# Kernel tuning notes

Measured on AMD Instinct MI355X. Metric: run time of the kernel, lower is better.

The kernel has to match this reference:

```python
import jax, jax.numpy as jnp
import numpy as np

N = 50000       # nodes
E = 1600000     # edges (avg degree 32)
D = 128         # in = hidden = out channels
H = 4           # attention heads


def setup_inputs() -> dict:
    key = jax.random.key(0)
    ks = jax.random.split(key, 9)
    s = 1.0 / np.sqrt(D)  # ~kaiming-scale linear weights
    return {
        "x": jax.random.normal(ks[0], (N, D), jnp.float32),
        "Wk": jax.random.normal(ks[1], (D, D), jnp.float32) * s,
        "bk": jnp.zeros((D,), jnp.float32),
        "Wq": jax.random.normal(ks[2], (D, D), jnp.float32) * s,
        "bq": jnp.zeros((D,), jnp.float32),
        "Wv": jax.random.normal(ks[3], (D, D), jnp.float32) * s,
        "bv": jnp.zeros((D,), jnp.float32),
        "src": jax.random.randint(ks[4], (E,), 0, N, dtype=jnp.int32),
        "dst": jax.random.randint(ks[5], (E,), 0, N, dtype=jnp.int32),
    }


def reference(x, Wk, bk, Wq, bq, Wv, bv, src, dst):
    n = x.shape[0]
    heads = H
    dk = Wk.shape[0] // heads
    dv = Wv.shape[0] // heads
    # Dense projections (near-roofline GEMMs)
    k = (x @ Wk.T + bk).reshape(n, heads, dk)
    q = (x @ Wq.T + bq).reshape(n, heads, dk)
    v = (x @ Wv.T + bv).reshape(n, heads, dv)
    # u_dot_v: per-edge per-head dot product (NO 1/sqrt(dk) scaling in source)
    scores = jnp.einsum('ehd,ehd->eh', k[src], q[dst])  # [E,H]
    # edge_softmax: softmax over incoming edges of each destination node
    m = jax.ops.segment_max(scores, dst, num_segments=n)        # [N,H]
    p = jnp.exp(scores - m[dst])                                 # [E,H]
    denom = jax.ops.segment_sum(p, dst, num_segments=n)         # [N,H]
    alpha = p / denom[dst]                                       # [E,H]
    # u_mul_e + sum: weighted scatter-aggregation of source values
    res = jax.ops.segment_sum(v[src] * alpha[:, :, None], dst, num_segments=n)  # [N,H,dv]
    # original: view(batch_size, -1, out_channels) with batch_size = N -> [N,1,out]
    return res.reshape(n, 1, heads * dv)
```

## Files before the change

### kernel.cpp

```cpp
#include <hip/hip_runtime.h>
#include <hip/hip_bf16.h>
#include <hip/hip_fp16.h>

#define NN 50000
#define NE 1600000
#define DD 128
#define HH 4
#define BSH2 5
#define NBKT2 1563
#define NBP2 2048
#define CAP 1408
#define PCHUNK 8192
#define NPB 196
#define NGB 560
#define MIDB (NGB + NPB)

typedef __attribute__((ext_vector_type(8))) short short8;
typedef __attribute__((ext_vector_type(4))) float floatx4;
typedef __attribute__((ext_vector_type(2))) _Float16 h2;

__device__ inline h2 as_h2(unsigned u) {
    union { unsigned u; h2 h; } c; c.u = u; return c.h;
}

__device__ inline float dot4(h2 a01, h2 a23, h2 b01, h2 b23) {
#if defined(__has_builtin) && __has_builtin(__builtin_amdgcn_fdot2)
    return __builtin_amdgcn_fdot2(a01, b01, __builtin_amdgcn_fdot2(a23, b23, 0.f, false), false);
#else
    return (float)a01.x * (float)b01.x + (float)a01.y * (float)b01.y +
           (float)a23.x * (float)b23.x + (float)a23.y * (float)b23.y;
#endif
}

__global__ __launch_bounds__(256) void prep_w(
    const float* __restrict__ Wk, const float* __restrict__ Wq, const float* __restrict__ Wv,
    unsigned short* __restrict__ hi, unsigned short* __restrict__ lo, int* __restrict__ bcur)
{
    int j = blockIdx.x * 256 + threadIdx.x;
    if (j < NBP2) bcur[j] = 0;
    if (j >= 3 * DD * DD) return;
    int which = j / (DD * DD);
    int off = j - which * (DD * DD);
    const float* W = (which == 0) ? Wk : (which == 1) ? Wq : Wv;
    float w = W[off];
    unsigned int b = __float_as_uint(w);
    unsigned short h = (unsigned short)(b >> 16);
    float hf = __uint_as_float((unsigned int)h << 16);
    float l = w - hf;
    hi[j] = h;
    lo[j] = (unsigned short)(__float_as_uint(l) >> 16);
}

__global__ __launch_bounds__(256) void mid(
    const float* __restrict__ x,
    const unsigned short* __restrict__ whi, const unsigned short* __restrict__ wlo,
    const float* __restrict__ bk, const float* __restrict__ bq, const float* __restrict__ bv,
    uint2* __restrict__ kv2, uint4* __restrict__ qh4,
    const int* __restrict__ src, const int* __restrict__ dst,
    int* __restrict__ bcur, int* __restrict__ epack)
{
    __shared__ __align__(16) unsigned char smem[49152];

    if (blockIdx.x < NGB) {
        uint4* wl4 = (uint4*)smem;
        int tid = threadIdx.x;
        int wave = tid >> 6, lane = tid & 63;
        int m = lane & 15, quad = lane >> 4;
        unsigned short* st = (unsigned short*)(smem + 32768 + wave * 4096);
        uint4* st4 = (uint4*)st;
        uint2* st2 = (uint2*)st;

        for (int pp = 0; pp < 3; ++pp) {
            int wm = (pp == 0) ? 0 : (pp == 1) ? 2 : 1;
            const uint4* gh = (const uint4*)whi + (size_t)wm * 2048;
            __syncthreads();
            for (int g = tid; g < 2048; g += 256) {
                int l = (g & ~15) | ((g ^ (g >> 4)) & 15);
                wl4[l] = gh[g];
            }
            __syncthreads();
            const unsigned short* wloP = wlo + (size_t)wm * (DD * DD);
            const float* bias = (pp == 0) ? bk : (pp == 1) ? bv : bq;
            float bs[8];
#pragma unroll
            for (int ct = 0; ct < 8; ++ct) bs[ct] = bias[ct * 16 + m];

            for (int tile = blockIdx.x * 4 + wave; tile < 3125; tile += NGB * 4) {
                int n0 = tile * 16;
                const float* xrow = x + (size_t)(n0 + m) * DD + quad * 8;
                short8 ah[4], al[4];
#pragma unroll
                for (int ks = 0; ks < 4; ++ks) {
                    const float* xr = xrow + ks * 32;
                    float4 t0 = *(const float4*)xr;
                    float4 t1 = *(const float4*)(xr + 4);
                    float xv[8] = {t0.x, t0.y, t0.z, t0.w, t1.x, t1.y, t1.z, t1.w};
#pragma unroll
                    for (int j = 0; j < 8; ++j) {
                        unsigned int b = __float_as_uint(xv[j]);
                        unsigned short h = (unsigned short)(b >> 16);
                        float hf = __uint_as_float((unsigned int)h << 16);
                        float l = xv[j] - hf;
                        ah[ks][j] = (short)h;
                        al[ks][j] = (short)(__float_as_uint(l) >> 16);
                    }
                }

                floatx4 acc[8];
#pragma unroll
                for (int ct = 0; ct < 8; ++ct) acc[ct] = (floatx4){0.f, 0.f, 0.f, 0.f};

#pragma unroll
                for (int ks = 0; ks < 4; ++ks) {
#pragma unroll
                    for (int ct = 0; ct < 8; ++ct) {
                        int r = ct * 16 + m;
                        short8 bh = ((const short8*)wl4)[r * 16 + ((ks * 4 + quad) ^ m)];
                        short8 bl = *(const short8*)(wloP + (size_t)r * 128 + ks * 32 + quad * 8);
                        acc[ct] = __builtin_amdgcn_mfma_f32_16x16x32_bf16(ah[ks], bh, acc[ct], 0, 0, 0);
                        acc[ct] = __builtin_amdgcn_mfma_f32_16x16x32_bf16(ah[ks], bl, acc[ct], 0, 0, 0);
                        acc[ct] = __builtin_amdgcn_mfma_f32_16x16x32_bf16(al[ks], bh, acc[ct], 0, 0, 0);
                    }
                }

#pragma unroll
                for (int ct = 0; ct < 8; ++ct) {
                    int j = ct * 16 + m;
#pragma unroll
                    for (int r = 0; r < 4; ++r)
                        st[(quad * 4 + r) * 128 + j] = __half_as_ushort(__float2half(acc[ct][r] + bs[ct]));
                }
                if (pp < 2) {
                    int voff = (pp == 1) ? 1 : 0;
#pragma unroll
                    for (int t = 0; t < 8; ++t) {
                        int flat = t * 64 + lane;
                        int row = flat >> 5, gg = flat & 31;
                        kv2[((size_t)(n0 + row)) * 64 + gg * 2 + voff] = st2[flat];
                    }
                } else {
#pragma unroll
                    for (int t = 0; t < 4; ++t) {
                        int flat = t * 64 + lane;
                        qh4[((size_t)(n0 + (flat >> 4))) * 16 + (flat & 15)] = st4[flat];
                    }
                }
            }
        }
    } else {
        int* h  = (int*)smem;
        int* c2 = h + NBP2;
        int pb = blockIdx.x - NGB;
        int b0 = pb * PCHUNK;
        int n = min(PCHUNK, NE - b0);
        for (int i = threadIdx.x; i < NBP2; i += 256) h[i] = 0;
        __syncthreads();
        for (int i = threadIdx.x; i < n; i += 256)
            atomicAdd(&h[dst[b0 + i] >> BSH2], 1);
        __syncthreads();
        for (int i = threadIdx.x; i < NBP2; i += 256)
            c2[i] = h[i] ? i * CAP + atomicAdd(&bcur[i], h[i]) : 0;
        __syncthreads();
        for (int i = threadIdx.x; i < n; i += 256) {
            int d = dst[b0 + i];
            int s = src[b0 + i];
            int bkt = d >> BSH2;
            int pos = atomicAdd(&c2[bkt], 1);
            if (pos < (bkt + 1) * CAP)
                epack[pos] = ((d & 31) << 16) | s;
        }
    }
}

__global__ __launch_bounds__(256) void gat_bucket(
    const __half* __restrict__ qh, const uint4* __restrict__ kvpack,
    const int* __restrict__ epack, const int* __restrict__ bcur,
    float* __restrict__ out)
{
    __shared__ int hist[32];
    __shared__ int cur[32];
    __shared__ int begs[33];
    __shared__ unsigned short els[CAP];
    int b = blockIdx.x;
    int cnt = min(bcur[b], CAP);
    int base = b * CAP;
    int n0 = b << BSH2;
    int nnodes = min(32, NN - n0);
    int tid = threadIdx.x;

    if (tid < 32) hist[tid] = 0;
    __syncthreads();
    for (int e = tid; e < cnt; e += 256)
        atomicAdd(&hist[epack[base + e] >> 16], 1);
    __syncthreads();
    if (tid < 32) {
        int c = hist[tid], inc = c;
#pragma unroll
        for (int d = 1; d < 32; d <<= 1) {
            int t = __shfl_up(inc, d);
            if (tid >= d) inc += t;
        }
        int excl = inc - c;
        begs[tid] = excl;
        cur[tid]  = excl;
        if (tid == 31) begs[32] = excl + c;
    }
    __syncthreads();
    for (int e = tid; e < cnt; e += 256) {
        int p = epack[base + e];
        int pos = atomicAdd(&cur[p >> 16], 1);
        els[pos] = (unsigned short)(p & 0xFFFF);
    }
    __syncthreads();

    int il = tid & 31;
    int hw = tid >> 5;
    const uint4* kvb = kvpack + il;

    for (int nl = hw; nl < nnodes; nl += 8) {
        int node = n0 + nl;
        int beg = begs[nl], end = begs[nl + 1];

        uint2 qq = *(const uint2*)(qh + (size_t)node * 128 + il * 4);
        h2 qh01 = as_h2(qq.x), qh23 = as_h2(qq.y);

        float m = -INFINITY, ssum = 0.f;
        float o0 = 0.f, o1 = 0.f, o2 = 0.f, o3 = 0.f;

        uint4 kvv[8];
        int nh = end - beg; if (nh > 8) nh = 8;
        if (nh > 0) {
#pragma unroll
            for (int i = 0; i < 8; ++i) {
                int s = els[beg + ((i < nh) ? i : 0)];
                kvv[i] = kvb[(size_t)s * 32];
            }
        }

        for (int j = beg; j < end; j += 8) {
            int jn = j + 8;
            int rem = end - jn;
            uint4 kvn[8];
            if (rem > 0) {
                int nhc = (rem > 8) ? 8 : rem;
#pragma unroll
                for (int i = 0; i < 8; ++i) {
                    int s = els[jn + ((i < nhc) ? i : 0)];
                    kvn[i] = kvb[(size_t)s * 32];
                }
            }
            float p[8];
#pragma unroll
            for (int i = 0; i < 8; ++i) {
                float t = dot4(as_h2(kvv[i].x), as_h2(kvv[i].y), qh01, qh23);
                t += __shfl_xor(t, 1);
                t += __shfl_xor(t, 2);
                t += __shfl_xor(t, 4);
                p[i] = (i < nh) ? t : -INFINITY;
            }
            float gm = fmaxf(fmaxf(fmaxf(p[0], p[1]), fmaxf(p[2], p[3])),
                             fmaxf(fmaxf(p[4], p[5]), fmaxf(p[6], p[7])));
            float nm = fmaxf(m, gm);
            float nmc = fmaxf(nm, -1e30f);
            float scale = __expf(m - nmc);
            ssum *= scale; o0 *= scale; o1 *= scale; o2 *= scale; o3 *= scale;
#pragma unroll
            for (int i = 0; i < 8; ++i) {
                float w = __expf(p[i] - nmc);
                ssum += w;
                o0 += w * (float)as_h2(kvv[i].z).x;
                o1 += w * (float)as_h2(kvv[i].z).y;
                o2 += w * (float)as_h2(kvv[i].w).x;
                o3 += w * (float)as_h2(kvv[i].w).y;
            }
            m = nm;
#pragma unroll
            for (int i = 0; i < 8; ++i) kvv[i] = kvn[i];
            nh = (rem > 8) ? 8 : rem;
        }

        float invd = (ssum > 0.f) ? 1.f / ssum : 0.f;
        float4 r = {o0 * invd, o1 * invd, o2 * invd, o3 * invd};
        *(float4*)(out + (size_t)node * DD + il * 4) = r;
    }
}

extern "C" void kernel_launch(void* const* d_in, const int* in_sizes, int n_in,
                              void* d_out, int out_size, void* d_ws, size_t ws_size,
                              hipStream_t stream) {
    const float* x  = (const float*)d_in[0];
    const float* Wk = (const float*)d_in[1];
    const float* bk = (const float*)d_in[2];
    const float* Wq = (const float*)d_in[3];
    const float* bq = (const float*)d_in[4];
    const float* Wv = (const float*)d_in[5];
    const float* bv = (const float*)d_in[6];
    const int* src = (const int*)d_in[7];
    const int* dst = (const int*)d_in[8];

    uint4*  kvpack = (uint4*)d_ws;
    __half* qh     = (__half*)(kvpack + (size_t)NN * 32);
    unsigned short* whi = (unsigned short*)(qh + (size_t)NN * DD);
    unsigned short* wlo = whi + (size_t)3 * DD * DD;
    int* epack = (int*)(wlo + (size_t)3 * DD * DD);
    int* bcur  = epack + (size_t)NBKT2 * CAP;

    prep_w<<<(3 * DD * DD + 255) / 256, 256, 0, stream>>>(Wk, Wq, Wv, whi, wlo, bcur);
    mid<<<MIDB, 256, 0, stream>>>(x, whi, wlo, bk, bq, bv, (uint2*)kvpack, (uint4*)qh,
                                  src, dst, bcur, epack);
    gat_bucket<<<NBKT2, 256, 0, stream>>>(qh, kvpack, epack, bcur, (float*)d_out);
}
```

Before: 291.3 us.

## Split fused projection/partition kernel and stage low-part weights in LDS

The fused kernel, which mixed GEMM blocks and edge-partition blocks in one launch, is split into separate partition and GEMM kernels on the same stream. The GEMM now stages both the high and low bf16 weight halves in shared memory (80KB LDS) instead of reading the low half from global memory inside the MFMA loop, with the grid reduced to 512 blocks. This removes the per-MFMA global loads but loses the concurrent overlap of partitioning with the GEMM, adds a kernel launch, and the larger LDS use may lower occupancy.

```diff
diff --git a/kernel.cpp b/kernel.cpp
--- a/kernel.cpp
+++ b/kernel.cpp
@@ -12,8 +12,7 @@
 #define CAP 1408
 #define PCHUNK 8192
 #define NPB 196
-#define NGB 560
-#define MIDB (NGB + NPB)
+#define GB 512
 
 typedef __attribute__((ext_vector_type(8))) short short8;
 typedef __attribute__((ext_vector_type(4))) float floatx4;
@@ -51,123 +50,127 @@
     lo[j] = (unsigned short)(__float_as_uint(l) >> 16);
 }
 
-__global__ __launch_bounds__(256) void mid(
+__global__ __launch_bounds__(256) void part(
+    const int* __restrict__ src, const int* __restrict__ dst,
+    int* __restrict__ bcur, int* __restrict__ epack)
+{
+    __shared__ int h[NBP2];
+    __shared__ int c2[NBP2];
+    int pb = blockIdx.x;
+    int b0 = pb * PCHUNK;
+    int n = min(PCHUNK, NE - b0);
+    for (int i = threadIdx.x; i < NBP2; i += 256) h[i] = 0;
+    __syncthreads();
+    for (int i = threadIdx.x; i < n; i += 256)
+        atomicAdd(&h[dst[b0 + i] >> BSH2], 1);
+    __syncthreads();
+    for (int i = threadIdx.x; i < NBP2; i += 256)
+        c2[i] = h[i] ? i * CAP + atomicAdd(&bcur[i], h[i]) : 0;
+    __syncthreads();
+    for (int i = threadIdx.x; i < n; i += 256) {
+        int d = dst[b0 + i];
+        int s = src[b0 + i];
+        int bkt = d >> BSH2;
+        int pos = atomicAdd(&c2[bkt], 1);
+        if (pos < (bkt + 1) * CAP)
+            epack[pos] = ((d & 31) << 16) | s;
+    }
+}
+
+__global__ __launch_bounds__(256) void gemm(
     const float* __restrict__ x,
     const unsigned short* __restrict__ whi, const unsigned short* __restrict__ wlo,
     const float* __restrict__ bk, const float* __restrict__ bq, const float* __restrict__ bv,
-    uint2* __restrict__ kv2, uint4* __restrict__ qh4,
-    const int* __restrict__ src, const int* __restrict__ dst,
-    int* __restrict__ bcur, int* __restrict__ epack)
+    uint2* __restrict__ kv2, uint4* __restrict__ qh4)
 {
-    __shared__ __align__(16) unsigned char smem[49152];
-
-    if (blockIdx.x < NGB) {
-        uint4* wl4 = (uint4*)smem;
-        int tid = threadIdx.x;
-        int wave = tid >> 6, lane = tid & 63;
-        int m = lane & 15, quad = lane >> 4;
-        unsigned short* st = (unsigned short*)(smem + 32768 + wave * 4096);
-        uint4* st4 = (uint4*)st;
-        uint2* st2 = (uint2*)st;
-
-        for (int pp = 0; pp < 3; ++pp) {
-            int wm = (pp == 0) ? 0 : (pp == 1) ? 2 : 1;
-            const uint4* gh = (const uint4*)whi + (size_t)wm * 2048;
-            __syncthreads();
-            for (int g = tid; g < 2048; g += 256) {
-                int l = (g & ~15) | ((g ^ (g >> 4)) & 15);
-                wl4[l] = gh[g];
-            }
-            __syncthreads();
-            const unsigned short* wloP = wlo + (size_t)wm * (DD * DD);
-            const float* bias = (pp == 0) ? bk : (pp == 1) ? bv : bq;
-            float bs[8];
-#pragma unroll
-            for (int ct = 0; ct < 8; ++ct) bs[ct] = bias[ct * 16 + m];
-
-            for (int tile = blockIdx.x * 4 + wave; tile < 3125; tile += NGB * 4) {
-                int n0 = tile * 16;
-                const float* xrow = x + (size_t)(n0 + m) * DD + quad * 8;
-                short8 ah[4], al[4];
-#pragma unroll
-                for (int ks = 0; ks < 4; ++ks) {
-                    const float* xr = xrow + ks * 32;
-                    float4 t0 = *(const float4*)xr;
-                    float4 t1 = *(const float4*)(xr + 4);
-                    float xv[8] = {t0.x, t0.y, t0.z, t0.w, t1.x, t1.y, t1.z, t1.w};
-#pragma unroll
-                    for (int j = 0; j < 8; ++j) {
-                        unsigned int b = __float_as_uint(xv[j]);
-                        unsigned short h = (unsigned short)(b >> 16);
-                        float hf = __uint_as_float((unsigned int)h << 16);
-                        float l = xv[j] - hf;
-                        ah[ks][j] = (short)h;
-                        al[ks][j] = (short)(__float_as_uint(l) >> 16);
-                    }
-                }
-
-                floatx4 acc[8];
-#pragma unroll
-                for (int ct = 0; ct < 8; ++ct) acc[ct] = (floatx4){0.f, 0.f, 0.f, 0.f};
-
-#pragma unroll
-                for (int ks = 0; ks < 4; ++ks) {
-#pragma unroll
-                    for (int ct = 0; ct < 8; ++ct) {
-                        int r = ct * 16 + m;
-                        short8 bh = ((const short8*)wl4)[r * 16 + ((ks * 4 + quad) ^ m)];
-                        short8 bl = *(const short8*)(wloP + (size_t)r * 128 + ks * 32 + quad * 8);
-                        acc[ct] = __builtin_amdgcn_mfma_f32_16x16x32_bf16(ah[ks], bh, acc[ct], 0, 0, 0);
-                        acc[ct] = __builtin_amdgcn_mfma_f32_16x16x32_bf16(ah[ks], bl, acc[ct], 0, 0, 0);
-                        acc[ct] = __builtin_amdgcn_mfma_f32_16x16x32_bf16(al[ks], bh, acc[ct], 0, 0, 0);
-                    }
-                }
-
+    __shared__ __align__(16) unsigned char smem[81920];
+
+    uint4* wh4 = (uint4*)smem;
+    uint4* wl4 = (uint4*)(smem + 32768);
+    int tid = threadIdx.x;
+    int wave = tid >> 6, lane = tid & 63;
+    int m = lane & 15, quad = lane >> 4;
+    unsigned short* st = (unsigned short*)(smem + 65536 + wave * 4096);
+    uint4* st4 = (uint4*)st;
+    uint2* st2 = (uint2*)st;
+
+    for (int pp = 0; pp < 3; ++pp) {
+        int wm = (pp == 0) ? 0 : (pp == 1) ? 2 : 1;
+        const uint4* gh = (const uint4*)whi + (size_t)wm * 2048;
+        const uint4* gl = (const uint4*)wlo + (size_t)wm * 2048;
+        __syncthreads();
+        for (int g = tid; g < 2048; g += 256) {
+            int l = (g & ~15) | ((g ^ (g >> 4)) & 15);
+            wh4[l] = gh[g];
+            wl4[l] = gl[g];
+        }
+        __syncthreads();
+        const float* bias = (pp == 0) ? bk : (pp == 1) ? bv : bq;
+        float bs[8];
+#pragma unroll
+        for (int ct = 0; ct < 8; ++ct) bs[ct] = bias[ct * 16 + m];
+
+        for (int tile = blockIdx.x * 4 + wave; tile < 3125; tile += GB * 4) {
+            int n0 = tile * 16;
+            const float* xrow = x + (size_t)(n0 + m) * DD + quad * 8;
+            short8 ah[4], al[4];
+#pragma unroll
+            for (int ks = 0; ks < 4; ++ks) {
+                const float* xr = xrow + ks * 32;
+                float4 t0 = *(const float4*)xr;
+                float4 t1 = *(const float4*)(xr + 4);
+                float xv[8] = {t0.x, t0.y, t0.z, t0.w, t1.x, t1.y, t1.z, t1.w};
+#pragma unroll
+                for (int j = 0; j < 8; ++j) {
+                    unsigned int b = __float_as_uint(xv[j]);
+                    unsigned short h = (unsigned short)(b >> 16);
+                    float hf = __uint_as_float((unsigned int)h << 16);
+                    float l = xv[j] - hf;
+                    ah[ks][j] = (short)h;
+                    al[ks][j] = (short)(__float_as_uint(l) >> 16);
+                }
+            }
+
+            floatx4 acc[8];
+#pragma unroll
+            for (int ct = 0; ct < 8; ++ct) acc[ct] = (floatx4){0.f, 0.f, 0.f, 0.f};
+
+#pragma unroll
+            for (int ks = 0; ks < 4; ++ks) {
 #pragma unroll
                 for (int ct = 0; ct < 8; ++ct) {
-                    int j = ct * 16 + m;
-#pragma unroll
-                    for (int r = 0; r < 4; ++r)
-                        st[(quad * 4 + r) * 128 + j] = __half_as_ushort(__float2half(acc[ct][r] + bs[ct]));
-                }
-                if (pp < 2) {
-                    int voff = (pp == 1) ? 1 : 0;
-#pragma unroll
-                    for (int t = 0; t < 8; ++t) {
-                        int flat = t * 64 + lane;
-                        int row = flat >> 5, gg = flat & 31;
-                        kv2[((size_t)(n0 + row)) * 64 + gg * 2 + voff] = st2[flat];
-                    }
-                } else {
-#pragma unroll
-                    for (int t = 0; t < 4; ++t) {
-                        int flat = t * 64 + lane;
-                        qh4[((size_t)(n0 + (flat >> 4))) * 16 + (flat & 15)] = st4[flat];
-                    }
-                }
-            }
-        }
-    } else {
-        int* h  = (int*)smem;
-        int* c2 = h + NBP2;
-        int pb = blockIdx.x - NGB;
-        int b0 = pb * PCHUNK;
-        int n = min(PCHUNK, NE - b0);
-        for (int i = threadIdx.x; i < NBP2; i += 256) h[i] = 0;
-        __syncthreads();
-        for (int i = threadIdx.x; i < n; i += 256)
-            atomicAdd(&h[dst[b0 + i] >> BSH2], 1);
-        __syncthreads();
-        for (int i = threadIdx.x; i < NBP2; i += 256)
-            c2[i] = h[i] ? i * CAP + atomicAdd(&bcur[i], h[i]) : 0;
-        __syncthreads();
-        for (int i = threadIdx.x; i < n; i += 256) {
-            int d = dst[b0 + i];
-            int s = src[b0 + i];
-            int bkt = d >> BSH2;
-            int pos = atomicAdd(&c2[bkt], 1);
-            if (pos < (bkt + 1) * CAP)
-                epack[pos] = ((d & 31) << 16) | s;
+                    int r = ct * 16 + m;
+                    int idx = r * 16 + ((ks * 4 + quad) ^ m);
+                    short8 bh = ((const short8*)wh4)[idx];
+                    short8 bl = ((const short8*)wl4)[idx];
+                    acc[ct] = __builtin_amdgcn_mfma_f32_16x16x32_bf16(ah[ks], bh, acc[ct], 0, 0, 0);
+                    acc[ct] = __builtin_amdgcn_mfma_f32_16x16x32_bf16(ah[ks], bl, acc[ct], 0, 0, 0);
+                    acc[ct] = __builtin_amdgcn_mfma_f32_16x16x32_bf16(al[ks], bh, acc[ct], 0, 0, 0);
+                }
+            }
+
+#pragma unroll
+            for (int ct = 0; ct < 8; ++ct) {
+                int j = ct * 16 + m;
+#pragma unroll
+                for (int r = 0; r < 4; ++r)
+                    st[(quad * 4 + r) * 128 + j] = __half_as_ushort(__float2half(acc[ct][r] + bs[ct]));
+            }
+            if (pp < 2) {
+                int voff = (pp == 1) ? 1 : 0;
+#pragma unroll
+                for (int t = 0; t < 8; ++t) {
+                    int flat = t * 64 + lane;
+                    int row = flat >> 5, gg = flat & 31;
+                    kv2[((size_t)(n0 + row)) * 64 + gg * 2 + voff] = st2[flat];
+                }
+            } else {
+#pragma unroll
+                for (int t = 0; t < 4; ++t) {
+                    int flat = t * 64 + lane;
+                    qh4[((size_t)(n0 + (flat >> 4))) * 16 + (flat & 15)] = st4[flat];
+                }
+            }
         }
     }
 }
@@ -305,8 +308,8 @@
     int* epack = (int*)(wlo + (size_t)3 * DD * DD);
     int* bcur  = epack + (size_t)NBKT2 * CAP;
 
-    prep_w<<<(3 * DD * DD + 255) / 256, 256, 0, stream>>>(Wk, Wq, Wv, whi, wlo, bcur);
-    mid<<<MIDB, 256, 0, stream>>>(x, whi, wlo, bk, bq, bv, (uint2*)kvpack, (uint4*)qh,
-                                  src, dst, bcur, epack);
+    prep_w<<<192, 256, 0, stream>>>(Wk, Wq, Wv, whi, wlo, bcur);
+    part<<<NPB, 256, 0, stream>>>(src, dst, bcur, epack);
+    gemm<<<GB, 256, 0, stream>>>(x, whi, wlo, bk, bq, bv, (uint2*)kvpack, (uint4*)qh);
     gat_bucket<<<NBKT2, 256, 0, stream>>>(qh, kvpack, epack, bcur, (float*)d_out);
 }
```

After: 294.5 us. No clear change (+1.1%).
